# Kernel optimization log

Hardware: AMD Instinct MI355X
Metric: run time of the kernel (lower is better)

Reference implementation:

```python
import jax, jax.numpy as jnp
import numpy as np

N_NODES = 100000
N_EDGES = 1600000
IN_FEATS, HIDDEN_FEATS, OUT_FEATS = 32, 64, 16


def setup_inputs() -> dict:
    key = jax.random.key(0)
    ks = jax.random.split(key, 8)
    return {
        "features": jax.random.normal(ks[0], (N_NODES, IN_FEATS), dtype=jnp.float32),
        "src": jax.random.randint(ks[1], (N_EDGES,), 0, N_NODES, dtype=jnp.int64),
        "dst": jax.random.randint(ks[2], (N_EDGES,), 0, N_NODES, dtype=jnp.int64),
        "W1_self": jax.random.normal(ks[3], (IN_FEATS, HIDDEN_FEATS), dtype=jnp.float32) * 0.1,
        "W1_neigh": jax.random.normal(ks[4], (IN_FEATS, HIDDEN_FEATS), dtype=jnp.float32) * 0.1,
        "b1": jnp.zeros((HIDDEN_FEATS,), dtype=jnp.float32),
        "W2_self": jax.random.normal(ks[5], (HIDDEN_FEATS, OUT_FEATS), dtype=jnp.float32) * 0.1,
        "W2_neigh": jax.random.normal(ks[6], (HIDDEN_FEATS, OUT_FEATS), dtype=jnp.float32) * 0.1,
        "b2": jnp.zeros((OUT_FEATS,), dtype=jnp.float32),
    }


def _sage_conv_mean(h, src, dst, n_nodes, W_self, W_neigh, b):
    # DGL SAGEConv(mean): gather src features to edges, mean-reduce at dst,
    # then fc_self(h) + fc_neigh(mean_neigh) + bias.
    ones = jnp.ones(src.shape, dtype=h.dtype)
    deg = jax.ops.segment_sum(ones, dst, num_segments=n_nodes)  # in-degree [N]
    agg = jax.ops.segment_sum(h[src], dst, num_segments=n_nodes)  # [N, d]
    mean_neigh = agg / jnp.maximum(deg, 1.0)[:, None]
    return h @ W_self + mean_neigh @ W_neigh + b


def reference(features, src, dst, W1_self, W1_neigh, b1, W2_self, W2_neigh, b2):
    n = features.shape[0]
    h = _sage_conv_mean(features, src, dst, n, W1_self, W1_neigh, b1)
    h = jax.nn.relu(h)
    # dropout is identity at inference (Keras call default training=False)
    out = _sage_conv_mean(h, src, dst, n, W2_self, W2_neigh, b2)
    return out
```

## Files before the change

### kernel.cpp

```cpp
#include <hip/hip_runtime.h>

#define N_NODES 100000
#define N_EDGES 1600000
#define IN_F 32
#define HID_F 64
#define OUT_F 16
#define BSIZE 512
#define NBKT 256
#define CAP 10240
#define CHUNK 4096
#define NBUCK ((N_NODES + BSIZE - 1) / BSIZE)
#define CAPN 48
#define APITCH 68

using f2v = __attribute__((ext_vector_type(2))) float;

#define ADDQ(s, Q) do { f2v p_; \
  p_ = __builtin_amdgcn_cvt_pk_f32_fp8((int)(Q).x, false); s[0] += p_[0]; s[1] += p_[1]; \
  p_ = __builtin_amdgcn_cvt_pk_f32_fp8((int)(Q).x, true);  s[2] += p_[0]; s[3] += p_[1]; \
  p_ = __builtin_amdgcn_cvt_pk_f32_fp8((int)(Q).y, false); s[4] += p_[0]; s[5] += p_[1]; \
  p_ = __builtin_amdgcn_cvt_pk_f32_fp8((int)(Q).y, true);  s[6] += p_[0]; s[7] += p_[1]; \
  p_ = __builtin_amdgcn_cvt_pk_f32_fp8((int)(Q).z, false); s[8] += p_[0]; s[9] += p_[1]; \
  p_ = __builtin_amdgcn_cvt_pk_f32_fp8((int)(Q).z, true);  s[10] += p_[0]; s[11] += p_[1]; \
  p_ = __builtin_amdgcn_cvt_pk_f32_fp8((int)(Q).w, false); s[12] += p_[0]; s[13] += p_[1]; \
  p_ = __builtin_amdgcn_cvt_pk_f32_fp8((int)(Q).w, true);  s[14] += p_[0]; s[15] += p_[1]; \
} while (0)

__global__ __launch_bounds__(NBKT) void cursor_init_kernel(int* __restrict__ cursor) {
  cursor[threadIdx.x] = threadIdx.x * CAP;
}

__global__ __launch_bounds__(512) void bucket_kernel(
    const int* __restrict__ src, const int* __restrict__ dst,
    const float4* __restrict__ featin, uint4* __restrict__ featfp8,
    int* __restrict__ cursor, unsigned* __restrict__ sorted) {
  __shared__ unsigned stage[CHUNK];
  __shared__ unsigned char sbkt[CHUNK];
  __shared__ int lcnt[NBKT], lscan[NBKT], gbase[NBKT];
  __shared__ int wsum[4];
  int t = threadIdx.x;

  {
    int gtid = blockIdx.x * 512 + t;
    if (gtid < N_NODES * IN_F / 16) {
      float4 a = featin[4 * gtid], bb = featin[4 * gtid + 1];
      float4 c4 = featin[4 * gtid + 2], d = featin[4 * gtid + 3];
      uint4 r;
      int w;
      w = __builtin_amdgcn_cvt_pk_fp8_f32(a.x, a.y, 0, false);
      w = __builtin_amdgcn_cvt_pk_fp8_f32(a.z, a.w, w, true);
      r.x = (unsigned)w;
      w = __builtin_amdgcn_cvt_pk_fp8_f32(bb.x, bb.y, 0, false);
      w = __builtin_amdgcn_cvt_pk_fp8_f32(bb.z, bb.w, w, true);
      r.y = (unsigned)w;
      w = __builtin_amdgcn_cvt_pk_fp8_f32(c4.x, c4.y, 0, false);
      w = __builtin_amdgcn_cvt_pk_fp8_f32(c4.z, c4.w, w, true);
      r.z = (unsigned)w;
      w = __builtin_amdgcn_cvt_pk_fp8_f32(d.x, d.y, 0, false);
      w = __builtin_amdgcn_cvt_pk_fp8_f32(d.z, d.w, w, true);
      r.w = (unsigned)w;
      featfp8[gtid] = r;
    }
  }

  if (t < NBKT) lcnt[t] = 0;
  __syncthreads();

  int base = blockIdx.x * CHUNK;
  unsigned mypk[CHUNK / 512];
  int myb[CHUNK / 512], myrank[CHUNK / 512];
#pragma unroll
  for (int i = 0; i < CHUNK / 512; ++i) {
    int e = base + t + 512 * i;
    if (e < N_EDGES) {
      unsigned s = (unsigned)src[e], d = (unsigned)dst[e];
      myb[i] = (int)(d >> 9);
      mypk[i] = (s << 9) | (d & 511u);
      myrank[i] = atomicAdd(&lcnt[myb[i]], 1);
    } else {
      myb[i] = -1;
    }
  }
  __syncthreads();

  int x = 0;
  if (t < NBKT) {
    x = lcnt[t];
#pragma unroll
    for (int off = 1; off < 64; off <<= 1) {
      int y = __shfl_up(x, off);
      if ((t & 63) >= off) x += y;
    }
    if ((t & 63) == 63) wsum[t >> 6] = x;
  }
  __syncthreads();
  if (t < NBKT) {
    int w = t >> 6, add = 0;
    if (w > 0) add += wsum[0];
    if (w > 1) add += wsum[1];
    if (w > 2) add += wsum[2];
    lscan[t] = x + add;
    gbase[t] = lcnt[t] ? atomicAdd(&cursor[t], lcnt[t]) : 0;
  }
  __syncthreads();

#pragma unroll
  for (int i = 0; i < CHUNK / 512; ++i) {
    if (myb[i] >= 0) {
      int slot = (lscan[myb[i]] - lcnt[myb[i]]) + myrank[i];
      stage[slot] = mypk[i];
      sbkt[slot] = (unsigned char)myb[i];
    }
  }
  __syncthreads();
  int nvalid = min(CHUNK, N_EDGES - base);
  for (int i = t; i < nvalid; i += 512) {
    unsigned p = stage[i];
    int b = (int)sbkt[i];
    int addr = gbase[b] + (i - (lscan[b] - lcnt[b]));
    sorted[addr] = p;
  }
}

__global__ __launch_bounds__(1024) void csr_kernel(
    const unsigned* __restrict__ sorted, const int* __restrict__ cursor,
    int* __restrict__ cnt, int* __restrict__ col) {
  __shared__ int lcnt[BSIZE];
  int t = threadIdx.x;
  int b = blockIdx.x;
  if (t < BSIZE) lcnt[t] = 0;
  __syncthreads();

  int base = b * CAP;
  int ne = cursor[b] - base;
  for (int i = t; i < ne; i += 1024) {
    unsigned p = sorted[base + i];
    int d = (int)(p & (BSIZE - 1));
    int r = atomicAdd(&lcnt[d], 1);
    if (r < CAPN) col[(b * BSIZE + d) * CAPN + r] = (int)(p >> 9);
  }
  __syncthreads();
  if (t < BSIZE) {
    int v = b * BSIZE + t;
    if (v < N_NODES) cnt[v] = lcnt[t];
  }
}

__global__ __launch_bounds__(256) void l1g_kernel(
    const float* __restrict__ feat, const uint4* __restrict__ featfp8,
    const int* __restrict__ cnt, const int* __restrict__ col,
    const float* __restrict__ W1s, const float* __restrict__ W1n,
    const float* __restrict__ b1,
    const float* __restrict__ W2n, const float* __restrict__ W2s,
    unsigned* __restrict__ t2f8, float* __restrict__ s2) {
  __shared__ float sA[64 * APITCH];
  __shared__ float sW[64 * 64];

  int t = threadIdx.x;
  int tile = blockIdx.x * 64;
  int nvalid = min(64, N_NODES - tile);

  const float4* Fg = (const float4*)(feat + (size_t)tile * IN_F);
  int lim = nvalid * 8;
  int fi0 = t, fi1 = t + 256;
  float4 fa0, fa1;
  if (fi0 < lim) fa0 = Fg[fi0];
  if (fi1 < lim) fa1 = Fg[fi1];
  float4 wv[4];
#pragma unroll
  for (int it = 0; it < 4; ++it) {
    int idx = t + 256 * it;
    int row = idx >> 4;
    const float4* srcw = (row < 32) ? (const float4*)W1s : (const float4*)W1n;
    wv[it] = srcw[(row & 31) * 16 + (idx & 15)];
  }

  {
    int nl = t >> 2, c = (t >> 1) & 1, hp = t & 1;
    int v = tile + nl;
    if (nl < nvalid) {
      int deg = cnt[v];
      int start = v * CAPN;
      int end = start + min(deg, CAPN);
      float s[16];
#pragma unroll
      for (int j = 0; j < 16; ++j) s[j] = 0.0f;
      int e = start + hp;
      for (; e + 6 < end; e += 8) {
        uint4 q0 = featfp8[col[e] * 2 + c];
        uint4 q1 = featfp8[col[e + 2] * 2 + c];
        uint4 q2 = featfp8[col[e + 4] * 2 + c];
        uint4 q3 = featfp8[col[e + 6] * 2 + c];
        ADDQ(s, q0);
        ADDQ(s, q1);
        ADDQ(s, q2);
        ADDQ(s, q3);
      }
      for (; e < end; e += 2) {
        uint4 q = featfp8[col[e] * 2 + c];
        ADDQ(s, q);
      }
#pragma unroll
      for (int j = 0; j < 16; ++j) s[j] += __shfl_xor(s[j], 1);
      float inv = 1.0f / fmaxf((float)deg, 1.0f);
      int j0 = 8 * hp;
#pragma unroll
      for (int j = 0; j < 8; ++j)
        sA[(32 + 16 * c + j0 + j) * APITCH + nl] = s[j0 + j] * inv;
    }
  }

  if (fi0 < lim) {
    int n = fi0 >> 3, c8 = fi0 & 7;
    sA[(4 * c8 + 0) * APITCH + n] = fa0.x;
    sA[(4 * c8 + 1) * APITCH + n] = fa0.y;
    sA[(4 * c8 + 2) * APITCH + n] = fa0.z;
    sA[(4 * c8 + 3) * APITCH + n] = fa0.w;
  }
  if (fi1 < lim) {
    int n = fi1 >> 3, c8 = fi1 & 7;
    sA[(4 * c8 + 0) * APITCH + n] = fa1.x;
    sA[(4 * c8 + 1) * APITCH + n] = fa1.y;
    sA[(4 * c8 + 2) * APITCH + n] = fa1.z;
    sA[(4 * c8 + 3) * APITCH + n] = fa1.w;
  }
  {
    float4* Ws = (float4*)sW;
#pragma unroll
    for (int it = 0; it < 4; ++it) Ws[t + 256 * it] = wv[it];
  }

  int tx = t & 15, ty = t >> 4;
  int n0 = 4 * ty, c0 = 4 * tx;
  float4 bb = ((const float4*)b1)[tx];
  __syncthreads();

  float acc[4][4];
#pragma unroll
  for (int i = 0; i < 4; ++i) { acc[i][0] = bb.x; acc[i][1] = bb.y; acc[i][2] = bb.z; acc[i][3] = bb.w; }
#pragma unroll 4
  for (int k = 0; k < 64; ++k) {
    float4 a = *(const float4*)&sA[k * APITCH + n0];
    float4 w = *(const float4*)&sW[k * 64 + c0];
    acc[0][0] += a.x * w.x; acc[0][1] += a.x * w.y; acc[0][2] += a.x * w.z; acc[0][3] += a.x * w.w;
    acc[1][0] += a.y * w.x; acc[1][1] += a.y * w.y; acc[1][2] += a.y * w.z; acc[1][3] += a.y * w.w;
    acc[2][0] += a.z * w.x; acc[2][1] += a.z * w.y; acc[2][2] += a.z * w.z; acc[2][3] += a.z * w.w;
    acc[3][0] += a.w * w.x; acc[3][1] += a.w * w.y; acc[3][2] += a.w * w.z; acc[3][3] += a.w * w.w;
  }
  __syncthreads();

#pragma unroll
  for (int jj = 0; jj < 4; ++jj) {
    float4 v;
    v.x = fmaxf(acc[0][jj], 0.0f);
    v.y = fmaxf(acc[1][jj], 0.0f);
    v.z = fmaxf(acc[2][jj], 0.0f);
    v.w = fmaxf(acc[3][jj], 0.0f);
    *(float4*)&sA[(c0 + jj) * APITCH + n0] = v;
  }
  {
    float4* Ws = (float4*)sW;
#pragma unroll
    for (int it = 0; it < 2; ++it) {
      int idx = t + 256 * it;
      int row = idx >> 3, ch = idx & 7;
      const float4* srcw = (ch < 4) ? (const float4*)W2n : (const float4*)W2s;
      Ws[row * 8 + ch] = srcw[row * 4 + (ch & 3)];
    }
  }
  __syncthreads();

  int c2 = 2 * tx;
  float a0 = 0.f, a1 = 0.f, b0 = 0.f, b1_ = 0.f, d0 = 0.f, d1 = 0.f, e0 = 0.f, e1 = 0.f;
#pragma unroll 4
  for (int k = 0; k < 64; ++k) {
    float4 a = *(const float4*)&sA[k * APITCH + n0];
    float2 w = *(const float2*)&sW[k * 32 + c2];
    a0 += a.x * w.x; a1 += a.x * w.y;
    b0 += a.y * w.x; b1_ += a.y * w.y;
    d0 += a.z * w.x; d1 += a.z * w.y;
    e0 += a.w * w.x; e1 += a.w * w.y;
  }
  {
    float rs[4][2] = {{a0, a1}, {b0, b1_}, {d0, d1}, {e0, e1}};
    int cc = c2 & 15;
#pragma unroll
    for (int i = 0; i < 4; ++i) {
      int v = tile + n0 + i;
      if (v < N_NODES) {
        if (c2 < 16) {
          int w = __builtin_amdgcn_cvt_pk_fp8_f32(rs[i][0], rs[i][1], 0, false);
          *(unsigned short*)((char*)t2f8 + (size_t)v * 16 + cc) = (unsigned short)w;
        } else {
          *(float2*)&s2[v * OUT_F + cc] = make_float2(rs[i][0], rs[i][1]);
        }
      }
    }
  }
}

__global__ __launch_bounds__(256) void gather2_final_kernel(
    const int* __restrict__ cnt, const int* __restrict__ col,
    const uint4* __restrict__ t2f8, const float* __restrict__ s2,
    const float* __restrict__ b2, float* __restrict__ out) {
  int g = blockIdx.x * 256 + threadIdx.x;
  int v = g >> 1, hp = g & 1;
  if (v >= N_NODES) return;
  int deg = cnt[v];
  int start = v * CAPN;
  int end = start + min(deg, CAPN);
  float s[16];
#pragma unroll
  for (int j = 0; j < 16; ++j) s[j] = 0.0f;
  int e = start + hp;
  for (; e + 6 < end; e += 8) {
    uint4 q0 = t2f8[col[e]];
    uint4 q1 = t2f8[col[e + 2]];
    uint4 q2 = t2f8[col[e + 4]];
    uint4 q3 = t2f8[col[e + 6]];
    ADDQ(s, q0);
    ADDQ(s, q1);
    ADDQ(s, q2);
    ADDQ(s, q3);
  }
  for (; e < end; e += 2) {
    uint4 q = t2f8[col[e]];
    ADDQ(s, q);
  }
#pragma unroll
  for (int j = 0; j < 16; ++j) s[j] += __shfl_xor(s[j], 1);
  float inv = 1.0f / fmaxf((float)deg, 1.0f);
  const float4* S = (const float4*)s2;
  const float4* B = (const float4*)b2;
  float4* O = (float4*)out;
#pragma unroll
  for (int i = 0; i < 2; ++i) {
    int ii = 2 * hp + i;
    float4 sv = S[v * 4 + ii];
    float4 bv = B[ii];
    float4 r;
    r.x = sv.x + bv.x + s[4 * ii + 0] * inv;
    r.y = sv.y + bv.y + s[4 * ii + 1] * inv;
    r.z = sv.z + bv.z + s[4 * ii + 2] * inv;
    r.w = sv.w + bv.w + s[4 * ii + 3] * inv;
    O[v * 4 + ii] = r;
  }
}

extern "C" void kernel_launch(void* const* d_in, const int* in_sizes, int n_in,
                              void* d_out, int out_size, void* d_ws, size_t ws_size,
                              hipStream_t stream) {
  const float* feat = (const float*)d_in[0];
  const int* src    = (const int*)d_in[1];
  const int* dst    = (const int*)d_in[2];
  const float* W1s  = (const float*)d_in[3];
  const float* W1n  = (const float*)d_in[4];
  const float* b1   = (const float*)d_in[5];
  const float* W2s  = (const float*)d_in[6];
  const float* W2n  = (const float*)d_in[7];
  const float* b2   = (const float*)d_in[8];
  float* out = (float*)d_out;

  const size_t N = N_NODES;
  const size_t SLAB = (size_t)NBUCK * CAP;
  int* cnt = (int*)d_ws;
  int* col = cnt + N + 16;
  unsigned* sorted = (unsigned*)(col + N * CAPN + 16);
  float* s2 = (float*)sorted;
  unsigned* featfp8 = (unsigned*)(sorted + SLAB + 16);
  unsigned* t2f8 = featfp8 + 8 * N;
  int* cursor = (int*)(t2f8 + 4 * N);

  cursor_init_kernel<<<1, NBKT, 0, stream>>>(cursor);
  bucket_kernel<<<(N_EDGES + CHUNK - 1) / CHUNK, 512, 0, stream>>>(
      src, dst, (const float4*)feat, (uint4*)featfp8, cursor, sorted);
  csr_kernel<<<NBUCK, 1024, 0, stream>>>(sorted, cursor, cnt, col);
  l1g_kernel<<<(N_NODES + 63) / 64, 256, 0, stream>>>(
      feat, (const uint4*)featfp8, cnt, col, W1s, W1n, b1, W2n, W2s, t2f8, s2);
  gather2_final_kernel<<<(2 * N_NODES + 255) / 256, 256, 0, stream>>>(
      cnt, col, (const uint4*)t2f8, s2, b2, out);
}
```

Baseline: 161.7 us.

## Fuse pipeline into two persistent kernels joined by software grid barriers

Merges the bucketing and CSR-building kernels into one launch, and the layer-1 transform and layer-2 gather into another. Inside each, an atomic-counter grid barrier replaces the kernel boundary. The layer-1 stage becomes a grid-stride loop over tiles with a fixed grid of 1024 blocks. This removes several launch gaps and tail drains. In exchange, every block must be co-resident for the barriers to avoid deadlock, and the barrier spin plus uneven tile counts per block add overhead.

```diff
diff --git a/kernel.cpp b/kernel.cpp
--- a/kernel.cpp
+++ b/kernel.cpp
@@ -10,8 +10,10 @@
 #define CAP 10240
 #define CHUNK 4096
 #define NBUCK ((N_NODES + BSIZE - 1) / BSIZE)
+#define NCHUNK ((N_EDGES + CHUNK - 1) / CHUNK)
 #define CAPN 48
 #define APITCH 68
+#define GRID3 1024
 
 using f2v = __attribute__((ext_vector_type(2))) float;
 
@@ -26,18 +28,36 @@
   p_ = __builtin_amdgcn_cvt_pk_f32_fp8((int)(Q).w, true);  s[14] += p_[0]; s[15] += p_[1]; \
 } while (0)
 
-__global__ __launch_bounds__(NBKT) void cursor_init_kernel(int* __restrict__ cursor) {
+__device__ __forceinline__ void grid_barrier(int* cnt, int* go, int nb) {
+  __threadfence();
+  __syncthreads();
+  if (threadIdx.x == 0) {
+    if (__hip_atomic_fetch_add(cnt, 1, __ATOMIC_ACQ_REL, __HIP_MEMORY_SCOPE_AGENT) == nb - 1) {
+      __hip_atomic_store(go, 1, __ATOMIC_RELEASE, __HIP_MEMORY_SCOPE_AGENT);
+    } else {
+      while (__hip_atomic_load(go, __ATOMIC_ACQUIRE, __HIP_MEMORY_SCOPE_AGENT) == 0) {
+        __builtin_amdgcn_s_sleep(2);
+      }
+    }
+  }
+  __syncthreads();
+}
+
+__global__ __launch_bounds__(NBKT) void init_kernel(int* __restrict__ cursor, int* __restrict__ bar) {
   cursor[threadIdx.x] = threadIdx.x * CAP;
+  if (threadIdx.x < 4) bar[threadIdx.x] = 0;
 }
 
-__global__ __launch_bounds__(512) void bucket_kernel(
+__global__ __launch_bounds__(512, 4) void bucketcsr_kernel(
     const int* __restrict__ src, const int* __restrict__ dst,
     const float4* __restrict__ featin, uint4* __restrict__ featfp8,
-    int* __restrict__ cursor, unsigned* __restrict__ sorted) {
+    int* __restrict__ cursor, unsigned* __restrict__ sorted,
+    int* __restrict__ cnt, int* __restrict__ col, int* __restrict__ bar) {
   __shared__ unsigned stage[CHUNK];
   __shared__ unsigned char sbkt[CHUNK];
   __shared__ int lcnt[NBKT], lscan[NBKT], gbase[NBKT];
   __shared__ int wsum[4];
+  __shared__ int dcnt[BSIZE];
   int t = threadIdx.x;
 
   {
@@ -120,230 +140,232 @@
     int addr = gbase[b] + (i - (lscan[b] - lcnt[b]));
     sorted[addr] = p;
   }
+
+  grid_barrier(&bar[0], &bar[1], NCHUNK);
+
+  int b = blockIdx.x;
+  if (b < NBUCK) {
+    dcnt[t] = 0;
+    __syncthreads();
+    int cbase = b * CAP;
+    int ne = cursor[b] - cbase;
+    for (int i = t; i < ne; i += 512) {
+      unsigned p = sorted[cbase + i];
+      int d = (int)(p & (BSIZE - 1));
+      int r = atomicAdd(&dcnt[d], 1);
+      if (r < CAPN) col[(b * BSIZE + d) * CAPN + r] = (int)(p >> 9);
+    }
+    __syncthreads();
+    int v = b * BSIZE + t;
+    if (v < N_NODES) cnt[v] = dcnt[t];
+  }
 }
 
-__global__ __launch_bounds__(1024) void csr_kernel(
-    const unsigned* __restrict__ sorted, const int* __restrict__ cursor,
-    int* __restrict__ cnt, int* __restrict__ col) {
-  __shared__ int lcnt[BSIZE];
-  int t = threadIdx.x;
-  int b = blockIdx.x;
-  if (t < BSIZE) lcnt[t] = 0;
-  __syncthreads();
-
-  int base = b * CAP;
-  int ne = cursor[b] - base;
-  for (int i = t; i < ne; i += 1024) {
-    unsigned p = sorted[base + i];
-    int d = (int)(p & (BSIZE - 1));
-    int r = atomicAdd(&lcnt[d], 1);
-    if (r < CAPN) col[(b * BSIZE + d) * CAPN + r] = (int)(p >> 9);
-  }
-  __syncthreads();
-  if (t < BSIZE) {
-    int v = b * BSIZE + t;
-    if (v < N_NODES) cnt[v] = lcnt[t];
-  }
-}
-
-__global__ __launch_bounds__(256) void l1g_kernel(
+__global__ __launch_bounds__(256, 4) void fused_kernel(
     const float* __restrict__ feat, const uint4* __restrict__ featfp8,
     const int* __restrict__ cnt, const int* __restrict__ col,
     const float* __restrict__ W1s, const float* __restrict__ W1n,
     const float* __restrict__ b1,
     const float* __restrict__ W2n, const float* __restrict__ W2s,
-    unsigned* __restrict__ t2f8, float* __restrict__ s2) {
+    unsigned* __restrict__ t2f8, float* __restrict__ s2,
+    const float* __restrict__ b2, float* __restrict__ out,
+    int* __restrict__ bar) {
   __shared__ float sA[64 * APITCH];
   __shared__ float sW[64 * 64];
 
   int t = threadIdx.x;
-  int tile = blockIdx.x * 64;
-  int nvalid = min(64, N_NODES - tile);
-
-  const float4* Fg = (const float4*)(feat + (size_t)tile * IN_F);
-  int lim = nvalid * 8;
-  int fi0 = t, fi1 = t + 256;
-  float4 fa0, fa1;
-  if (fi0 < lim) fa0 = Fg[fi0];
-  if (fi1 < lim) fa1 = Fg[fi1];
-  float4 wv[4];
-#pragma unroll
-  for (int it = 0; it < 4; ++it) {
-    int idx = t + 256 * it;
-    int row = idx >> 4;
-    const float4* srcw = (row < 32) ? (const float4*)W1s : (const float4*)W1n;
-    wv[it] = srcw[(row & 31) * 16 + (idx & 15)];
-  }
-
-  {
-    int nl = t >> 2, c = (t >> 1) & 1, hp = t & 1;
-    int v = tile + nl;
-    if (nl < nvalid) {
-      int deg = cnt[v];
-      int start = v * CAPN;
-      int end = start + min(deg, CAPN);
-      float s[16];
-#pragma unroll
-      for (int j = 0; j < 16; ++j) s[j] = 0.0f;
-      int e = start + hp;
-      for (; e + 6 < end; e += 8) {
-        uint4 q0 = featfp8[col[e] * 2 + c];
-        uint4 q1 = featfp8[col[e + 2] * 2 + c];
-        uint4 q2 = featfp8[col[e + 4] * 2 + c];
-        uint4 q3 = featfp8[col[e + 6] * 2 + c];
-        ADDQ(s, q0);
-        ADDQ(s, q1);
-        ADDQ(s, q2);
-        ADDQ(s, q3);
+  const int NT = (N_NODES + 63) / 64;
+
+  for (int tile_i = blockIdx.x; tile_i < NT; tile_i += GRID3) {
+    __syncthreads();
+    int tile = tile_i * 64;
+    int nvalid = min(64, N_NODES - tile);
+
+    const float4* Fg = (const float4*)(feat + (size_t)tile * IN_F);
+    int lim = nvalid * 8;
+    int fi0 = t, fi1 = t + 256;
+    float4 fa0, fa1;
+    if (fi0 < lim) fa0 = Fg[fi0];
+    if (fi1 < lim) fa1 = Fg[fi1];
+    float4 wv[4];
+#pragma unroll
+    for (int it = 0; it < 4; ++it) {
+      int idx = t + 256 * it;
+      int row = idx >> 4;
+      const float4* srcw = (row < 32) ? (const float4*)W1s : (const float4*)W1n;
+      wv[it] = srcw[(row & 31) * 16 + (idx & 15)];
+    }
+
+    {
+      int nl = t >> 2, c = (t >> 1) & 1, hp = t & 1;
+      int v = tile + nl;
+      if (nl < nvalid) {
+        int deg = cnt[v];
+        int start = v * CAPN;
+        int end = start + min(deg, CAPN);
+        float s[16];
+#pragma unroll
+        for (int j = 0; j < 16; ++j) s[j] = 0.0f;
+        int e = start + hp;
+        for (; e + 6 < end; e += 8) {
+          uint4 q0 = featfp8[col[e] * 2 + c];
+          uint4 q1 = featfp8[col[e + 2] * 2 + c];
+          uint4 q2 = featfp8[col[e + 4] * 2 + c];
+          uint4 q3 = featfp8[col[e + 6] * 2 + c];
+          ADDQ(s, q0);
+          ADDQ(s, q1);
+          ADDQ(s, q2);
+          ADDQ(s, q3);
+        }
+        for (; e < end; e += 2) {
+          uint4 q = featfp8[col[e] * 2 + c];
+          ADDQ(s, q);
+        }
+#pragma unroll
+        for (int j = 0; j < 16; ++j) s[j] += __shfl_xor(s[j], 1);
+        float inv = 1.0f / fmaxf((float)deg, 1.0f);
+        int j0 = 8 * hp;
+#pragma unroll
+        for (int j = 0; j < 8; ++j)
+          sA[(32 + 16 * c + j0 + j) * APITCH + nl] = s[j0 + j] * inv;
       }
-      for (; e < end; e += 2) {
-        uint4 q = featfp8[col[e] * 2 + c];
-        ADDQ(s, q);
+    }
+
+    if (fi0 < lim) {
+      int n = fi0 >> 3, c8 = fi0 & 7;
+      sA[(4 * c8 + 0) * APITCH + n] = fa0.x;
+      sA[(4 * c8 + 1) * APITCH + n] = fa0.y;
+      sA[(4 * c8 + 2) * APITCH + n] = fa0.z;
+      sA[(4 * c8 + 3) * APITCH + n] = fa0.w;
+    }
+    if (fi1 < lim) {
+      int n = fi1 >> 3, c8 = fi1 & 7;
+      sA[(4 * c8 + 0) * APITCH + n] = fa1.x;
+      sA[(4 * c8 + 1) * APITCH + n] = fa1.y;
+      sA[(4 * c8 + 2) * APITCH + n] = fa1.z;
+      sA[(4 * c8 + 3) * APITCH + n] = fa1.w;
+    }
+    {
+      float4* Ws = (float4*)sW;
+#pragma unroll
+      for (int it = 0; it < 4; ++it) Ws[t + 256 * it] = wv[it];
+    }
+
+    int tx = t & 15, ty = t >> 4;
+    int n0 = 4 * ty, c0 = 4 * tx;
+    float4 bb = ((const float4*)b1)[tx];
+    __syncthreads();
+
+    float acc[4][4];
+#pragma unroll
+    for (int i = 0; i < 4; ++i) { acc[i][0] = bb.x; acc[i][1] = bb.y; acc[i][2] = bb.z; acc[i][3] = bb.w; }
+#pragma unroll 4
+    for (int k = 0; k < 64; ++k) {
+      float4 a = *(const float4*)&sA[k * APITCH + n0];
+      float4 w = *(const float4*)&sW[k * 64 + c0];
+      acc[0][0] += a.x * w.x; acc[0][1] += a.x * w.y; acc[0][2] += a.x * w.z; acc[0][3] += a.x * w.w;
+      acc[1][0] += a.y * w.x; acc[1][1] += a.y * w.y; acc[1][2] += a.y * w.z; acc[1][3] += a.y * w.w;
+      acc[2][0] += a.z * w.x; acc[2][1] += a.z * w.y; acc[2][2] += a.z * w.z; acc[2][3] += a.z * w.w;
+      acc[3][0] += a.w * w.x; acc[3][1] += a.w * w.y; acc[3][2] += a.w * w.z; acc[3][3] += a.w * w.w;
+    }
+    __syncthreads();
+
+#pragma unroll
+    for (int jj = 0; jj < 4; ++jj) {
+      float4 v;
+      v.x = fmaxf(acc[0][jj], 0.0f);
+      v.y = fmaxf(acc[1][jj], 0.0f);
+      v.z = fmaxf(acc[2][jj], 0.0f);
+      v.w = fmaxf(acc[3][jj], 0.0f);
+      *(float4*)&sA[(c0 + jj) * APITCH + n0] = v;
+    }
+    {
+      float4* Ws = (float4*)sW;
+#pragma unroll
+      for (int it = 0; it < 2; ++it) {
+        int idx = t + 256 * it;
+        int row = idx >> 3, ch = idx & 7;
+        const float4* srcw = (ch < 4) ? (const float4*)W2n : (const float4*)W2s;
+        Ws[row * 8 + ch] = srcw[row * 4 + (ch & 3)];
       }
-#pragma unroll
-      for (int j = 0; j < 16; ++j) s[j] += __shfl_xor(s[j], 1);
-      float inv = 1.0f / fmaxf((float)deg, 1.0f);
-      int j0 = 8 * hp;
-#pragma unroll
-      for (int j = 0; j < 8; ++j)
-        sA[(32 + 16 * c + j0 + j) * APITCH + nl] = s[j0 + j] * inv;
-    }
-  }
-
-  if (fi0 < lim) {
-    int n = fi0 >> 3, c8 = fi0 & 7;
-    sA[(4 * c8 + 0) * APITCH + n] = fa0.x;
-    sA[(4 * c8 + 1) * APITCH + n] = fa0.y;
-    sA[(4 * c8 + 2) * APITCH + n] = fa0.z;
-    sA[(4 * c8 + 3) * APITCH + n] = fa0.w;
-  }
-  if (fi1 < lim) {
-    int n = fi1 >> 3, c8 = fi1 & 7;
-    sA[(4 * c8 + 0) * APITCH + n] = fa1.x;
-    sA[(4 * c8 + 1) * APITCH + n] = fa1.y;
-    sA[(4 * c8 + 2) * APITCH + n] = fa1.z;
-    sA[(4 * c8 + 3) * APITCH + n] = fa1.w;
-  }
-  {
-    float4* Ws = (float4*)sW;
-#pragma unroll
-    for (int it = 0; it < 4; ++it) Ws[t + 256 * it] = wv[it];
-  }
-
-  int tx = t & 15, ty = t >> 4;
-  int n0 = 4 * ty, c0 = 4 * tx;
-  float4 bb = ((const float4*)b1)[tx];
-  __syncthreads();
-
-  float acc[4][4];
-#pragma unroll
-  for (int i = 0; i < 4; ++i) { acc[i][0] = bb.x; acc[i][1] = bb.y; acc[i][2] = bb.z; acc[i][3] = bb.w; }
+    }
+    __syncthreads();
+
+    int c2 = 2 * tx;
+    float a0 = 0.f, a1 = 0.f, b0 = 0.f, b1_ = 0.f, d0 = 0.f, d1 = 0.f, e0 = 0.f, e1 = 0.f;
 #pragma unroll 4
-  for (int k = 0; k < 64; ++k) {
-    float4 a = *(const float4*)&sA[k * APITCH + n0];
-    float4 w = *(const float4*)&sW[k * 64 + c0];
-    acc[0][0] += a.x * w.x; acc[0][1] += a.x * w.y; acc[0][2] += a.x * w.z; acc[0][3] += a.x * w.w;
-    acc[1][0] += a.y * w.x; acc[1][1] += a.y * w.y; acc[1][2] += a.y * w.z; acc[1][3] += a.y * w.w;
-    acc[2][0] += a.z * w.x; acc[2][1] += a.z * w.y; acc[2][2] += a.z * w.z; acc[2][3] += a.z * w.w;
-    acc[3][0] += a.w * w.x; acc[3][1] += a.w * w.y; acc[3][2] += a.w * w.z; acc[3][3] += a.w * w.w;
-  }
-  __syncthreads();
-
-#pragma unroll
-  for (int jj = 0; jj < 4; ++jj) {
-    float4 v;
-    v.x = fmaxf(acc[0][jj], 0.0f);
-    v.y = fmaxf(acc[1][jj], 0.0f);
-    v.z = fmaxf(acc[2][jj], 0.0f);
-    v.w = fmaxf(acc[3][jj], 0.0f);
-    *(float4*)&sA[(c0 + jj) * APITCH + n0] = v;
-  }
-  {
-    float4* Ws = (float4*)sW;
-#pragma unroll
-    for (int it = 0; it < 2; ++it) {
-      int idx = t + 256 * it;
-      int row = idx >> 3, ch = idx & 7;
-      const float4* srcw = (ch < 4) ? (const float4*)W2n : (const float4*)W2s;
-      Ws[row * 8 + ch] = srcw[row * 4 + (ch & 3)];
-    }
-  }
-  __syncthreads();
-
-  int c2 = 2 * tx;
-  float a0 = 0.f, a1 = 0.f, b0 = 0.f, b1_ = 0.f, d0 = 0.f, d1 = 0.f, e0 = 0.f, e1 = 0.f;
-#pragma unroll 4
-  for (int k = 0; k < 64; ++k) {
-    float4 a = *(const float4*)&sA[k * APITCH + n0];
-    float2 w = *(const float2*)&sW[k * 32 + c2];
-    a0 += a.x * w.x; a1 += a.x * w.y;
-    b0 += a.y * w.x; b1_ += a.y * w.y;
-    d0 += a.z * w.x; d1 += a.z * w.y;
-    e0 += a.w * w.x; e1 += a.w * w.y;
-  }
-  {
-    float rs[4][2] = {{a0, a1}, {b0, b1_}, {d0, d1}, {e0, e1}};
-    int cc = c2 & 15;
-#pragma unroll
-    for (int i = 0; i < 4; ++i) {
-      int v = tile + n0 + i;
-      if (v < N_NODES) {
-        if (c2 < 16) {
-          int w = __builtin_amdgcn_cvt_pk_fp8_f32(rs[i][0], rs[i][1], 0, false);
-          *(unsigned short*)((char*)t2f8 + (size_t)v * 16 + cc) = (unsigned short)w;
-        } else {
-          *(float2*)&s2[v * OUT_F + cc] = make_float2(rs[i][0], rs[i][1]);
+    for (int k = 0; k < 64; ++k) {
+      float4 a = *(const float4*)&sA[k * APITCH + n0];
+      float2 w = *(const float2*)&sW[k * 32 + c2];
+      a0 += a.x * w.x; a1 += a.x * w.y;
+      b0 += a.y * w.x; b1_ += a.y * w.y;
+      d0 += a.z * w.x; d1 += a.z * w.y;
+      e0 += a.w * w.x; e1 += a.w * w.y;
+    }
+    {
+      float rs[4][2] = {{a0, a1}, {b0, b1_}, {d0, d1}, {e0, e1}};
+      int cc = c2 & 15;
+#pragma unroll
+      for (int i = 0; i < 4; ++i) {
+        int v = tile + n0 + i;
+        if (v < N_NODES) {
+          if (c2 < 16) {
+            int w = __builtin_amdgcn_cvt_pk_fp8_f32(rs[i][0], rs[i][1], 0, false);
+            *(unsigned short*)((char*)t2f8 + (size_t)v * 16 + cc) = (unsigned short)w;
+          } else {
+            *(float2*)&s2[v * OUT_F + cc] = make_float2(rs[i][0], rs[i][1]);
+          }
         }
       }
     }
   }
-}
-
-__global__ __launch_bounds__(256) void gather2_final_kernel(
-    const int* __restrict__ cnt, const int* __restrict__ col,
-    const uint4* __restrict__ t2f8, const float* __restrict__ s2,
-    const float* __restrict__ b2, float* __restrict__ out) {
-  int g = blockIdx.x * 256 + threadIdx.x;
-  int v = g >> 1, hp = g & 1;
-  if (v >= N_NODES) return;
-  int deg = cnt[v];
-  int start = v * CAPN;
-  int end = start + min(deg, CAPN);
-  float s[16];
-#pragma unroll
-  for (int j = 0; j < 16; ++j) s[j] = 0.0f;
-  int e = start + hp;
-  for (; e + 6 < end; e += 8) {
-    uint4 q0 = t2f8[col[e]];
-    uint4 q1 = t2f8[col[e + 2]];
-    uint4 q2 = t2f8[col[e + 4]];
-    uint4 q3 = t2f8[col[e + 6]];
-    ADDQ(s, q0);
-    ADDQ(s, q1);
-    ADDQ(s, q2);
-    ADDQ(s, q3);
-  }
-  for (; e < end; e += 2) {
-    uint4 q = t2f8[col[e]];
-    ADDQ(s, q);
-  }
-#pragma unroll
-  for (int j = 0; j < 16; ++j) s[j] += __shfl_xor(s[j], 1);
-  float inv = 1.0f / fmaxf((float)deg, 1.0f);
-  const float4* S = (const float4*)s2;
-  const float4* B = (const float4*)b2;
-  float4* O = (float4*)out;
-#pragma unroll
-  for (int i = 0; i < 2; ++i) {
-    int ii = 2 * hp + i;
-    float4 sv = S[v * 4 + ii];
-    float4 bv = B[ii];
-    float4 r;
-    r.x = sv.x + bv.x + s[4 * ii + 0] * inv;
-    r.y = sv.y + bv.y + s[4 * ii + 1] * inv;
-    r.z = sv.z + bv.z + s[4 * ii + 2] * inv;
-    r.w = sv.w + bv.w + s[4 * ii + 3] * inv;
-    O[v * 4 + ii] = r;
+
+  grid_barrier(&bar[2], &bar[3], GRID3);
+
+  {
+    const uint4* T2 = (const uint4*)t2f8;
+    int g = blockIdx.x * 256 + t;
+    int v = g >> 1, hp = g & 1;
+    if (v >= N_NODES) return;
+    int deg = cnt[v];
+    int start = v * CAPN;
+    int end = start + min(deg, CAPN);
+    float s[16];
+#pragma unroll
+    for (int j = 0; j < 16; ++j) s[j] = 0.0f;
+    int e = start + hp;
+    for (; e + 6 < end; e += 8) {
+      uint4 q0 = T2[col[e]];
+      uint4 q1 = T2[col[e + 2]];
+      uint4 q2 = T2[col[e + 4]];
+      uint4 q3 = T2[col[e + 6]];
+      ADDQ(s, q0);
+      ADDQ(s, q1);
+      ADDQ(s, q2);
+      ADDQ(s, q3);
+    }
+    for (; e < end; e += 2) {
+      uint4 q = T2[col[e]];
+      ADDQ(s, q);
+    }
+#pragma unroll
+    for (int j = 0; j < 16; ++j) s[j] += __shfl_xor(s[j], 1);
+    float inv = 1.0f / fmaxf((float)deg, 1.0f);
+    const float4* S = (const float4*)s2;
+    const float4* B = (const float4*)b2;
+    float4* O = (float4*)out;
+#pragma unroll
+    for (int i = 0; i < 2; ++i) {
+      int ii = 2 * hp + i;
+      float4 sv = S[v * 4 + ii];
+      float4 bv = B[ii];
+      float4 r;
+      r.x = sv.x + bv.x + s[4 * ii + 0] * inv;
+      r.y = sv.y + bv.y + s[4 * ii + 1] * inv;
+      r.z = sv.z + bv.z + s[4 * ii + 2] * inv;
+      r.w = sv.w + bv.w + s[4 * ii + 3] * inv;
+      O[v * 4 + ii] = r;
+    }
   }
 }
 
@@ -370,13 +392,12 @@
   unsigned* featfp8 = (unsigned*)(sorted + SLAB + 16);
   unsigned* t2f8 = featfp8 + 8 * N;
   int* cursor = (int*)(t2f8 + 4 * N);
-
-  cursor_init_kernel<<<1, NBKT, 0, stream>>>(cursor);
-  bucket_kernel<<<(N_EDGES + CHUNK - 1) / CHUNK, 512, 0, stream>>>(
-      src, dst, (const float4*)feat, (uint4*)featfp8, cursor, sorted);
-  csr_kernel<<<NBUCK, 1024, 0, stream>>>(sorted, cursor, cnt, col);
-  l1g_kernel<<<(N_NODES + 63) / 64, 256, 0, stream>>>(
-      feat, (const uint4*)featfp8, cnt, col, W1s, W1n, b1, W2n, W2s, t2f8, s2);
-  gather2_final_kernel<<<(2 * N_NODES + 255) / 256, 256, 0, stream>>>(
-      cnt, col, (const uint4*)t2f8, s2, b2, out);
+  int* bar = cursor + NBKT;
+
+  init_kernel<<<1, NBKT, 0, stream>>>(cursor, bar);
+  bucketcsr_kernel<<<NCHUNK, 512, 0, stream>>>(
+      src, dst, (const float4*)feat, (uint4*)featfp8, cursor, sorted, cnt, col, bar);
+  fused_kernel<<<GRID3, 256, 0, stream>>>(
+      feat, (const uint4*)featfp8, cnt, col, W1s, W1n, b1, W2n, W2s,
+      t2f8, s2, b2, out, bar);
 }
```

Result: slower. 593.0 us (+266.8%).

## Split CSR build across more blocks with global atomics and vectorize column loads

Applied to the files above, without the earlier changes.

The CSR build now uses four 256-thread blocks per bucket instead of one 1024-thread block. Degrees are counted with global atomics on cnt, which the bucket kernel now zeroes up front. Both gather kernels load neighbor indices as int4 groups per half-pair instead of strided scalar loads. This buys more CSR parallelism and fewer index load instructions, at the cost of global atomic contention and a different edge order within each node's column list.

```diff
diff --git a/kernel.cpp b/kernel.cpp
--- a/kernel.cpp
+++ b/kernel.cpp
@@ -33,13 +33,18 @@
 __global__ __launch_bounds__(512) void bucket_kernel(
     const int* __restrict__ src, const int* __restrict__ dst,
     const float4* __restrict__ featin, uint4* __restrict__ featfp8,
-    int* __restrict__ cursor, unsigned* __restrict__ sorted) {
+    int* __restrict__ cursor, unsigned* __restrict__ sorted,
+    uint4* __restrict__ cnt4) {
   __shared__ unsigned stage[CHUNK];
   __shared__ unsigned char sbkt[CHUNK];
   __shared__ int lcnt[NBKT], lscan[NBKT], gbase[NBKT];
   __shared__ int wsum[4];
   int t = threadIdx.x;
 
+  {
+    int z = blockIdx.x * 512 + t;
+    if (z < N_NODES / 4) cnt4[z] = make_uint4(0u, 0u, 0u, 0u);
+  }
   {
     int gtid = blockIdx.x * 512 + t;
     if (gtid < N_NODES * IN_F / 16) {
@@ -122,27 +127,19 @@
   }
 }
 
-__global__ __launch_bounds__(1024) void csr_kernel(
+__global__ __launch_bounds__(256) void csr_kernel(
     const unsigned* __restrict__ sorted, const int* __restrict__ cursor,
     int* __restrict__ cnt, int* __restrict__ col) {
-  __shared__ int lcnt[BSIZE];
-  int t = threadIdx.x;
-  int b = blockIdx.x;
-  if (t < BSIZE) lcnt[t] = 0;
-  __syncthreads();
-
-  int base = b * CAP;
-  int ne = cursor[b] - base;
-  for (int i = t; i < ne; i += 1024) {
-    unsigned p = sorted[base + i];
-    int d = (int)(p & (BSIZE - 1));
-    int r = atomicAdd(&lcnt[d], 1);
-    if (r < CAPN) col[(b * BSIZE + d) * CAPN + r] = (int)(p >> 9);
-  }
-  __syncthreads();
-  if (t < BSIZE) {
-    int v = b * BSIZE + t;
-    if (v < N_NODES) cnt[v] = lcnt[t];
+  int j = blockIdx.x;
+  int b = j >> 2, q = j & 3;
+  int cbase = b * CAP;
+  int ne = cursor[b] - cbase;
+  int lo = (ne * q) >> 2, hi = (ne * (q + 1)) >> 2;
+  for (int i = lo + (int)threadIdx.x; i < hi; i += 256) {
+    unsigned p = sorted[cbase + i];
+    int v = b * BSIZE + (int)(p & (BSIZE - 1));
+    int r = atomicAdd(&cnt[v], 1);
+    if (r < CAPN) col[v * CAPN + r] = (int)(p >> 9);
   }
 }
 
@@ -181,22 +178,24 @@
     if (nl < nvalid) {
       int deg = cnt[v];
       int start = v * CAPN;
-      int end = start + min(deg, CAPN);
+      int dclamp = min(deg, CAPN);
+      int end = start + dclamp;
       float s[16];
 #pragma unroll
       for (int j = 0; j < 16; ++j) s[j] = 0.0f;
-      int e = start + hp;
-      for (; e + 6 < end; e += 8) {
-        uint4 q0 = featfp8[col[e] * 2 + c];
-        uint4 q1 = featfp8[col[e + 2] * 2 + c];
-        uint4 q2 = featfp8[col[e + 4] * 2 + c];
-        uint4 q3 = featfp8[col[e + 6] * 2 + c];
+      int nf = dclamp & ~7;
+      for (int g = 0; g < nf; g += 8) {
+        int4 cc = *(const int4*)&col[start + g + 4 * hp];
+        uint4 q0 = featfp8[cc.x * 2 + c];
+        uint4 q1 = featfp8[cc.y * 2 + c];
+        uint4 q2 = featfp8[cc.z * 2 + c];
+        uint4 q3 = featfp8[cc.w * 2 + c];
         ADDQ(s, q0);
         ADDQ(s, q1);
         ADDQ(s, q2);
         ADDQ(s, q3);
       }
-      for (; e < end; e += 2) {
+      for (int e = start + nf + hp; e < end; e += 2) {
         uint4 q = featfp8[col[e] * 2 + c];
         ADDQ(s, q);
       }
@@ -308,22 +307,24 @@
   if (v >= N_NODES) return;
   int deg = cnt[v];
   int start = v * CAPN;
-  int end = start + min(deg, CAPN);
+  int dclamp = min(deg, CAPN);
+  int end = start + dclamp;
   float s[16];
 #pragma unroll
   for (int j = 0; j < 16; ++j) s[j] = 0.0f;
-  int e = start + hp;
-  for (; e + 6 < end; e += 8) {
-    uint4 q0 = t2f8[col[e]];
-    uint4 q1 = t2f8[col[e + 2]];
-    uint4 q2 = t2f8[col[e + 4]];
-    uint4 q3 = t2f8[col[e + 6]];
+  int nf = dclamp & ~7;
+  for (int gg = 0; gg < nf; gg += 8) {
+    int4 cc = *(const int4*)&col[start + gg + 4 * hp];
+    uint4 q0 = t2f8[cc.x];
+    uint4 q1 = t2f8[cc.y];
+    uint4 q2 = t2f8[cc.z];
+    uint4 q3 = t2f8[cc.w];
     ADDQ(s, q0);
     ADDQ(s, q1);
     ADDQ(s, q2);
     ADDQ(s, q3);
   }
-  for (; e < end; e += 2) {
+  for (int e = start + nf + hp; e < end; e += 2) {
     uint4 q = t2f8[col[e]];
     ADDQ(s, q);
   }
@@ -373,8 +374,8 @@
 
   cursor_init_kernel<<<1, NBKT, 0, stream>>>(cursor);
   bucket_kernel<<<(N_EDGES + CHUNK - 1) / CHUNK, 512, 0, stream>>>(
-      src, dst, (const float4*)feat, (uint4*)featfp8, cursor, sorted);
-  csr_kernel<<<NBUCK, 1024, 0, stream>>>(sorted, cursor, cnt, col);
+      src, dst, (const float4*)feat, (uint4*)featfp8, cursor, sorted, (uint4*)cnt);
+  csr_kernel<<<NBUCK * 4, 256, 0, stream>>>(sorted, cursor, cnt, col);
   l1g_kernel<<<(N_NODES + 63) / 64, 256, 0, stream>>>(
       feat, (const uint4*)featfp8, cnt, col, W1s, W1n, b1, W2n, W2s, t2f8, s2);
   gather2_final_kernel<<<(2 * N_NODES + 255) / 256, 256, 0, stream>>>(
```

After: 200.3 us. 1.24x slower.
